# Performance work log

Measured on AMD Instinct MI355X. Metric: run time of the kernel, lower is better.

The kernel has to match this reference:

```python
import jax, jax.numpy as jnp
import numpy as np

N = 20000   # nodes
E = 320000  # edges
H = 4       # attention heads
GAT_SLOPE = 0.2   # DGL GATv2Conv internal leaky_relu slope
ACT_SLOPE = 0.01  # nn.LeakyReLU default slope


def gatv2_layer(h, src, dst, Wl, Wr, attn, b):
    """DGL GATv2Conv (share_weights=False, bias=True, eval mode).
    h: [N, Fin]; Wl/Wr: [Fin, H*D]; attn: [H, D]; b: [H*D]. Returns [N, H, D]."""
    n = h.shape[0]
    Hh, D = attn.shape
    fs = (h @ Wl).reshape(n, Hh, D)  # source projection
    fd = (h @ Wr).reshape(n, Hh, D)  # destination projection
    # edge-wise GATv2 score: a^T leaky_relu(Wl h_u + Wr h_v)
    e = jax.nn.leaky_relu(fs[src] + fd[dst], negative_slope=GAT_SLOPE)  # [E,H,D]
    logit = jnp.einsum('ehd,hd->eh', e, attn)  # [E,H]
    # edge softmax over incoming edges of each dst node (numerically stable)
    m = jax.ops.segment_max(logit, dst, num_segments=n)
    a = jnp.exp(logit - m[dst])
    s = jax.ops.segment_sum(a, dst, num_segments=n)
    alpha = a / s[dst]  # [E,H]
    out = jax.ops.segment_sum(alpha[:, :, None] * fs[src], dst, num_segments=n)
    return out + b.reshape(1, Hh, D)


def setup_inputs() -> dict:
    key = jax.random.key(0)
    ks = jax.random.split(key, 16)

    def w(k, shape, fan_in):
        return (jax.random.normal(k, shape, jnp.float32) / np.float32(np.sqrt(fan_in)))

    return {
        'n_feat': jax.random.normal(ks[0], (N, 512), jnp.float32),
        'src': jax.random.randint(ks[1], (E,), 0, N, jnp.int32),
        'dst': jax.random.randint(ks[2], (E,), 0, N, jnp.int32),
        # layer 0: 512 -> H x 128
        'Wl0': w(ks[3], (512, H * 128), 512), 'Wr0': w(ks[4], (512, H * 128), 512),
        'attn0': w(ks[5], (H, 128), 128), 'b0': jnp.zeros((H * 128,), jnp.float32),
        # layer 1: 128 -> H x 128
        'Wl1': w(ks[6], (128, H * 128), 128), 'Wr1': w(ks[7], (128, H * 128), 128),
        'attn1': w(ks[8], (H, 128), 128), 'b1': jnp.zeros((H * 128,), jnp.float32),
        # layer 2 (output): 128 -> H x 64
        'Wl2': w(ks[9], (128, H * 64), 128), 'Wr2': w(ks[10], (128, H * 64), 128),
        'attn2': w(ks[11], (H, 64), 64), 'b2': jnp.zeros((H * 64,), jnp.float32),
    }


def reference(n_feat, src, dst, Wl0, Wr0, attn0, b0, Wl1, Wr1, attn1, b1,
              Wl2, Wr2, attn2, b2):
    h = n_feat.reshape(n_feat.shape[0], -1)  # nn.Flatten
    for (Wl, Wr, attn, b) in ((Wl0, Wr0, attn0, b0),
                              (Wl1, Wr1, attn1, b1),
                              (Wl2, Wr2, attn2, b2)):
        h = gatv2_layer(h, src, dst, Wl, Wr, attn, b)  # [N,H,D]
        h = h.mean(axis=1)                              # head mean
        h = jax.nn.leaky_relu(h, negative_slope=ACT_SLOPE)
    # dgl.mean_nodes: per-graph mean readout (single graph -> [1, out])
    return h.mean(axis=0, keepdims=True)
```

## Files before the change

### kernel.cpp

```cpp
#include <hip/hip_runtime.h>
#include <hip/hip_bf16.h>
#include <stdint.h>


#define GAT_SLOPE 0.2f
#define ACT_SLOPE 0.01f
#define MAXDEG 64

typedef _Float16 half8 __attribute__((ext_vector_type(8)));
typedef _Float16 v2h __attribute__((ext_vector_type(2)));
typedef float floatx4 __attribute__((ext_vector_type(4)));

struct TransDesc {
  const float* src;
  _Float16* dst;
  int K, M, off;
};
struct PreArgs {
  TransDesc d[6];
  int wTotal;
  const float* nf;
  _Float16* A0;
  int aTotal;
  const int* src;
  const int* dst;
  int* counts;
  int* pcsrc;
  int E;
};

__global__ __launch_bounds__(256) void preproc_kernel(PreArgs pa) {
  int i = blockIdx.x * 256 + threadIdx.x;
  const int total = pa.wTotal + pa.aTotal + pa.E;
  if (i >= total) return;
  if (i < pa.wTotal) {
    int q = 0;
#pragma unroll
    for (int j = 1; j < 6; ++j)
      if (i >= pa.d[j].off) q = j;
    int local = i - pa.d[q].off;
    int K = pa.d[q].K, M = pa.d[q].M;
    int m = local / K, k = local % K;
    pa.d[q].dst[local] = (_Float16)pa.d[q].src[(size_t)k * M + m];
  } else if (i < pa.wTotal + pa.aTotal) {
    int j = i - pa.wTotal;
    pa.A0[j] = (_Float16)pa.nf[j];
  } else {
    int e = i - pa.wTotal - pa.aTotal;
    int d = pa.dst[e];
    int pos = atomicAdd(&pa.counts[d], 1);
    if (pos < MAXDEG) pa.pcsrc[(size_t)d * MAXDEG + pos] = pa.src[e];
  }
}

__device__ __forceinline__ void gload_lds16(const _Float16* g, _Float16* l) {
  __builtin_amdgcn_global_load_lds(
      (__attribute__((address_space(1))) unsigned int*)g,
      (__attribute__((address_space(3))) unsigned int*)l, 16, 0, 0);
}

#define TM 128
#define TN 128
#define TK 32

__global__ __launch_bounds__(256) void gemm_mfma_dual_kernel(
    const _Float16* __restrict__ A, const _Float16* __restrict__ B0,
    const _Float16* __restrict__ B1, _Float16* __restrict__ C0,
    _Float16* __restrict__ C1, int Nrow, int K, int M, int nStrips,
    int nbxLog2) {
  const int id = blockIdx.x;
  const int xcd = id & 7;
  const int s = id >> 3;
  const int nbx = 1 << nbxLog2;
  const int col = s & (nbx - 1);
  const int chunk = s >> nbxLog2;
  const int strip = chunk * 8 + xcd;
  if (strip >= nStrips) return;

  const int nb = nbx >> 1;
  const bool second = col >= nb;
  const _Float16* B = second ? B1 : B0;
  _Float16* C = second ? C1 : C0;
  const int bn = (second ? col - nb : col) * TN;
  const int bm = strip * TM;

  __shared__ __align__(16) _Float16 As[TM * TK];
  __shared__ __align__(16) _Float16 Bs[TN * TK];

  const int tid = threadIdx.x;
  const int w = tid >> 6;
  const int lane = tid & 63;
  const int wr = w >> 1;
  const int wc = w & 1;
  const int quad = lane >> 4;
  const int lr = lane & 15;

  const int lrow = lane >> 2;
  const int loff = (lane & 3) * 8;

  floatx4 acc[4][4];
#pragma unroll
  for (int i = 0; i < 4; ++i)
#pragma unroll
    for (int j = 0; j < 4; ++j) acc[i][j] = (floatx4){0.f, 0.f, 0.f, 0.f};

  const int KT = K / TK;
  for (int kt = 0; kt < KT; ++kt) {
    const int k0 = kt * TK;
#pragma unroll
    for (int half = 0; half < 2; ++half) {
      const int r0 = w * 32 + half * 16;
      int ga = bm + r0 + lrow;
      if (ga >= Nrow) ga = Nrow - 1;
      gload_lds16(A + (size_t)ga * K + k0 + loff, As + r0 * TK);
      gload_lds16(B + (size_t)(bn + r0 + lrow) * K + k0 + loff, Bs + r0 * TK);
    }
    __syncthreads();

    half8 ar[4], br[4];
#pragma unroll
    for (int i = 0; i < 4; ++i) {
      int row = wr * 64 + i * 16 + lr;
      ar[i] = *(const half8*)(As + row * TK + quad * 8);
    }
#pragma unroll
    for (int j = 0; j < 4; ++j) {
      int colr = wc * 64 + j * 16 + lr;
      br[j] = *(const half8*)(Bs + colr * TK + quad * 8);
    }
#pragma unroll
    for (int i = 0; i < 4; ++i)
#pragma unroll
      for (int j = 0; j < 4; ++j)
        acc[i][j] = __builtin_amdgcn_mfma_f32_16x16x32_f16(ar[i], br[j],
                                                           acc[i][j], 0, 0, 0);
    __syncthreads();
  }

#pragma unroll
  for (int i = 0; i < 4; ++i) {
#pragma unroll
    for (int r = 0; r < 4; ++r) {
      int row = bm + wr * 64 + i * 16 + quad * 4 + r;
      if (row >= Nrow) continue;
#pragma unroll
      for (int j = 0; j < 4; ++j) {
        int colc = bn + wc * 64 + j * 16 + lr;
        C[(size_t)row * M + colc] = (_Float16)acc[i][j][r];
      }
    }
  }
}

template <int D>
__global__ __launch_bounds__(128) void node_attn_kernel(
    const _Float16* __restrict__ fs, const _Float16* __restrict__ fd,
    const int* __restrict__ counts, const int* __restrict__ pcsrc,
    const float* __restrict__ attn, const float* __restrict__ bias,
    float* __restrict__ hout, _Float16* __restrict__ oh, int N) {
  constexpr int HD = 4 * D;
  constexpr int R = HD / 64;
  constexpr int R2 = R / 2;
  typedef _Float16 halfR __attribute__((ext_vector_type(R)));
  union Frag {
    halfR v;
    v2h h[R2];
    _Float16 s[R];
  };
  const int v = blockIdx.x;
  if (v >= N) return;
  const int wid = threadIdx.x >> 6;
  const int lane = threadIdx.x & 63;

  const v2h slope2 = {(_Float16)GAT_SLOPE, (_Float16)GAT_SLOPE};

  Frag fdv;
  fdv.v = *(const halfR*)(fd + (size_t)v * HD + lane * R);
  v2h ar2[R2];
#pragma unroll
  for (int j = 0; j < R2; ++j) {
    ar2[j][0] = (_Float16)attn[lane * R + 2 * j];
    ar2[j][1] = (_Float16)attn[lane * R + 2 * j + 1];
  }

  float m = -INFINITY, l = 0.f;
  float O[R];
#pragma unroll
  for (int i = 0; i < R; ++i) O[i] = 0.f;

  const int cnt = min(counts[v], MAXDEG);
  const int* elist = pcsrc + (size_t)v * MAXDEG;
  const int mid = (cnt + 1) >> 1;
  int k = wid ? mid : 0;
  const int ke = wid ? cnt : mid;

  for (; k + 3 < ke; k += 4) {
    const int s0 = elist[k];
    const int s1 = elist[k + 1];
    const int s2 = elist[k + 2];
    const int s3 = elist[k + 3];
    Frag t0, t1, t2, t3;
    t0.v = *(const halfR*)(fs + (size_t)s0 * HD + lane * R);
    t1.v = *(const halfR*)(fs + (size_t)s1 * HD + lane * R);
    t2.v = *(const halfR*)(fs + (size_t)s2 * HD + lane * R);
    t3.v = *(const halfR*)(fs + (size_t)s3 * HD + lane * R);
    float p0 = 0.f, p1 = 0.f, p2 = 0.f, p3 = 0.f;
#pragma unroll
    for (int j = 0; j < R2; ++j) {
      v2h x0 = t0.h[j] + fdv.h[j];
      v2h x1 = t1.h[j] + fdv.h[j];
      v2h x2 = t2.h[j] + fdv.h[j];
      v2h x3 = t3.h[j] + fdv.h[j];
      x0 = __builtin_elementwise_max(x0, x0 * slope2);
      x1 = __builtin_elementwise_max(x1, x1 * slope2);
      x2 = __builtin_elementwise_max(x2, x2 * slope2);
      x3 = __builtin_elementwise_max(x3, x3 * slope2);
      p0 = __builtin_amdgcn_fdot2(ar2[j], x0, p0, false);
      p1 = __builtin_amdgcn_fdot2(ar2[j], x1, p1, false);
      p2 = __builtin_amdgcn_fdot2(ar2[j], x2, p2, false);
      p3 = __builtin_amdgcn_fdot2(ar2[j], x3, p3, false);
    }
#pragma unroll
    for (int off = 1; off <= 8; off <<= 1) {
      p0 += __shfl_xor(p0, off, 64);
      p1 += __shfl_xor(p1, off, 64);
      p2 += __shfl_xor(p2, off, 64);
      p3 += __shfl_xor(p3, off, 64);
    }
    const float mq = fmaxf(fmaxf(p0, p1), fmaxf(p2, p3));
    const float w0 = __expf(p0 - mq);
    const float w1 = __expf(p1 - mq);
    const float w2 = __expf(p2 - mq);
    const float w3 = __expf(p3 - mq);
    const float mnew = fmaxf(m, mq);
    const float sc = __expf(m - mnew);
    const float sq = __expf(mq - mnew);
    l = l * sc + (w0 + w1 + w2 + w3) * sq;
#pragma unroll
    for (int i = 0; i < R; ++i) {
      float acc = (float)t0.s[i] * w0;
      acc = fmaf((float)t1.s[i], w1, acc);
      acc = fmaf((float)t2.s[i], w2, acc);
      acc = fmaf((float)t3.s[i], w3, acc);
      O[i] = fmaf(O[i], sc, sq * acc);
    }
    m = mnew;
  }
  for (; k < ke; ++k) {
    const int s0 = elist[k];
    Frag t0;
    t0.v = *(const halfR*)(fs + (size_t)s0 * HD + lane * R);
    float p0 = 0.f;
#pragma unroll
    for (int j = 0; j < R2; ++j) {
      v2h x0 = t0.h[j] + fdv.h[j];
      x0 = __builtin_elementwise_max(x0, x0 * slope2);
      p0 = __builtin_amdgcn_fdot2(ar2[j], x0, p0, false);
    }
#pragma unroll
    for (int off = 1; off <= 8; off <<= 1) p0 += __shfl_xor(p0, off, 64);
    const float mnew = fmaxf(m, p0);
    const float sc = __expf(m - mnew);
    const float p = __expf(p0 - mnew);
    l = l * sc + p;
#pragma unroll
    for (int i = 0; i < R; ++i) O[i] = fmaf(O[i], sc, p * (float)t0.s[i]);
    m = mnew;
  }

  __shared__ float sO[64 * R];
  __shared__ float sM[64];
  __shared__ float sL[64];
  if (wid == 1) {
    sM[lane] = m;
    sL[lane] = l;
#pragma unroll
    for (int i = 0; i < R; ++i) sO[lane * R + i] = O[i];
  }
  __syncthreads();
  if (wid == 1) return;
  {
    const float m1 = sM[lane];
    const float l1 = sL[lane];
    const float mstar = fmaxf(m, m1);
    const float a0 = (l > 0.f) ? __expf(m - mstar) : 0.f;
    const float a1 = (l1 > 0.f) ? __expf(m1 - mstar) : 0.f;
    l = l * a0 + l1 * a1;
#pragma unroll
    for (int i = 0; i < R; ++i) O[i] = O[i] * a0 + sO[lane * R + i] * a1;
  }

  const float inv = (l > 0.f) ? 1.f / l : 0.f;
#pragma unroll
  for (int i = 0; i < R; ++i) O[i] = O[i] * inv + bias[lane * R + i];
#pragma unroll
  for (int i = 0; i < R; ++i) {
    O[i] += __shfl_xor(O[i], 16, 64);
    O[i] += __shfl_xor(O[i], 32, 64);
    float x = O[i] * 0.25f;
    O[i] = x > 0.f ? x : x * ACT_SLOPE;
  }
  if (lane < 16) {
    const size_t base = (size_t)v * D + lane * R;
    if (hout) {
#pragma unroll
      for (int i = 0; i < R; ++i) hout[base + i] = O[i];
    }
    if (oh) {
#pragma unroll
      for (int i = 0; i < R; ++i) oh[base + i] = (_Float16)O[i];
    }
  }
}

__global__ __launch_bounds__(64) void final_mean_kernel(
    const float* __restrict__ h, float* __restrict__ out, int N) {
  const int d = threadIdx.x;
  float acc = 0.f;
  for (int n = blockIdx.x; n < N; n += gridDim.x) acc += h[(size_t)n * 64 + d];
  atomicAdd(&out[d], acc / (float)N);
}

extern "C" void kernel_launch(void* const* d_in, const int* in_sizes, int n_in,
                              void* d_out, int out_size, void* d_ws,
                              size_t ws_size, hipStream_t stream) {
  const float* n_feat = (const float*)d_in[0];
  const int* src = (const int*)d_in[1];
  const int* dst = (const int*)d_in[2];
  const float* Wl[3] = {(const float*)d_in[3], (const float*)d_in[7],
                        (const float*)d_in[11]};
  const float* Wr[3] = {(const float*)d_in[4], (const float*)d_in[8],
                        (const float*)d_in[12]};
  const float* attn[3] = {(const float*)d_in[5], (const float*)d_in[9],
                          (const float*)d_in[13]};
  const float* bias[3] = {(const float*)d_in[6], (const float*)d_in[10],
                          (const float*)d_in[14]};

  const int N = in_sizes[0] / 512;
  const int E = in_sizes[1];
  const int Kdim[3] = {512, 128, 128};
  const int Mdim[3] = {512, 512, 256};

  char* ws = (char*)d_ws;
  size_t o = 0;
  auto alloc = [&](size_t bytes) {
    void* p = ws + o;
    o += (bytes + 15) & ~(size_t)15;
    return p;
  };
  _Float16* fs = (_Float16*)alloc((size_t)N * 512 * 2);
  _Float16* fd = (_Float16*)alloc((size_t)N * 512 * 2);
  _Float16* A0 = (_Float16*)alloc((size_t)N * 512 * 2);
  _Float16* h1 = (_Float16*)alloc((size_t)N * 128 * 2);
  _Float16* h2 = (_Float16*)alloc((size_t)N * 128 * 2);
  float* hfin = (float*)alloc((size_t)N * 64 * 4);
  _Float16 *WlT[3], *WrT[3];
  for (int L = 0; L < 3; ++L) {
    size_t sz = (size_t)Kdim[L] * Mdim[L] * 2;
    WlT[L] = (_Float16*)alloc(sz);
    WrT[L] = (_Float16*)alloc(sz);
  }
  int* counts = (int*)alloc((size_t)N * 4);
  int* pcsrc = (int*)alloc((size_t)N * MAXDEG * 4);

  hipMemsetAsync(counts, 0, (size_t)N * sizeof(int), stream);
  {
    PreArgs pa;
    int off = 0;
    for (int L = 0; L < 3; ++L) {
      pa.d[2 * L] = {Wl[L], WlT[L], Kdim[L], Mdim[L], off};
      off += Kdim[L] * Mdim[L];
      pa.d[2 * L + 1] = {Wr[L], WrT[L], Kdim[L], Mdim[L], off};
      off += Kdim[L] * Mdim[L];
    }
    pa.wTotal = off;
    pa.nf = n_feat;
    pa.A0 = A0;
    pa.aTotal = N * 512;
    pa.src = src;
    pa.dst = dst;
    pa.counts = counts;
    pa.pcsrc = pcsrc;
    pa.E = E;
    int total = pa.wTotal + pa.aTotal + pa.E;
    preproc_kernel<<<(total + 255) / 256, 256, 0, stream>>>(pa);
  }

  const _Float16* Ain[3] = {A0, h1, h2};

  const int nStrips = (N + TM - 1) / TM;
  const int S8 = ((nStrips + 7) / 8) * 8;

  for (int L = 0; L < 3; ++L) {
    const int K = Kdim[L], M = Mdim[L];
    const int nbx = 2 * M / TN;
    const int nbxLog2 = (nbx == 8) ? 3 : 2;
    gemm_mfma_dual_kernel<<<S8 * nbx, 256, 0, stream>>>(
        Ain[L], WlT[L], WrT[L], fs, fd, N, K, M, nStrips, nbxLog2);
    if (L == 0) {
      node_attn_kernel<128><<<N, 128, 0, stream>>>(fs, fd, counts, pcsrc,
                                                   attn[L], bias[L], nullptr,
                                                   h1, N);
    } else if (L == 1) {
      node_attn_kernel<128><<<N, 128, 0, stream>>>(fs, fd, counts, pcsrc,
                                                   attn[L], bias[L], nullptr,
                                                   h2, N);
    } else {
      node_attn_kernel<64><<<N, 128, 0, stream>>>(fs, fd, counts, pcsrc,
                                                  attn[L], bias[L], hfin,
                                                  nullptr, N);
    }
  }

  hipMemsetAsync(d_out, 0, 64 * sizeof(float), stream);
  final_mean_kernel<<<256, 64, 0, stream>>>(hfin, (float*)d_out, N);
}
```

Baseline: 357.6 us.

## Fuse whole GATv2 pipeline into one cooperative persistent kernel with grid syncs

Replaces the separate preprocess, GEMM, attention and final-mean launches with a single cooperative mega-kernel whose stages are separated by grid.sync, with the counts and output zeroing folded into the preprocessing stage instead of memsets. The attention stage now handles one node per wave (four per block) instead of splitting one node across two waves, and the last layer reduces the node mean into shared memory and atomics, dropping the hfin buffer and the final kernel. The aim is to remove launch gaps and intermediate traffic. In exchange the GEMM and attention stages run on a fixed persistent grid capped at 768 blocks, and grid-wide barriers add sync cost. A multi-kernel fallback path is kept.

```diff
diff --git a/kernel.cpp b/kernel.cpp
--- a/kernel.cpp
+++ b/kernel.cpp
@@ -1,23 +1,26 @@
 #include <hip/hip_runtime.h>
+#include <hip/hip_cooperative_groups.h>
 #include <hip/hip_bf16.h>
 #include <stdint.h>
+
+namespace cg = cooperative_groups;
 
 
 #define GAT_SLOPE 0.2f
 #define ACT_SLOPE 0.01f
 #define MAXDEG 64
+#define TM 128
+#define TN 128
+#define TK 32
 
 typedef _Float16 half8 __attribute__((ext_vector_type(8)));
 typedef _Float16 v2h __attribute__((ext_vector_type(2)));
 typedef float floatx4 __attribute__((ext_vector_type(4)));
 
-struct TransDesc {
-  const float* src;
-  _Float16* dst;
-  int K, M, off;
-};
-struct PreArgs {
-  TransDesc d[6];
+struct MegaArgs {
+  const float* W[6];
+  _Float16* WT[6];
+  int wK[6], wM[6], wOff[6];
   int wTotal;
   const float* nf;
   _Float16* A0;
@@ -27,31 +30,19 @@
   int* counts;
   int* pcsrc;
   int E;
+  float* dout;
+  const _Float16* Ain[3];
+  const _Float16* Bl[3];
+  const _Float16* Br[3];
+  _Float16* fs;
+  _Float16* fd;
+  _Float16* oh[2];
+  const float* aw[3];
+  const float* bias[3];
+  int Kd[3], Md[3], tiles[3], nbxL[3];
+  int nStrips;
+  int N;
 };
-
-__global__ __launch_bounds__(256) void preproc_kernel(PreArgs pa) {
-  int i = blockIdx.x * 256 + threadIdx.x;
-  const int total = pa.wTotal + pa.aTotal + pa.E;
-  if (i >= total) return;
-  if (i < pa.wTotal) {
-    int q = 0;
-#pragma unroll
-    for (int j = 1; j < 6; ++j)
-      if (i >= pa.d[j].off) q = j;
-    int local = i - pa.d[q].off;
-    int K = pa.d[q].K, M = pa.d[q].M;
-    int m = local / K, k = local % K;
-    pa.d[q].dst[local] = (_Float16)pa.d[q].src[(size_t)k * M + m];
-  } else if (i < pa.wTotal + pa.aTotal) {
-    int j = i - pa.wTotal;
-    pa.A0[j] = (_Float16)pa.nf[j];
-  } else {
-    int e = i - pa.wTotal - pa.aTotal;
-    int d = pa.dst[e];
-    int pos = atomicAdd(&pa.counts[d], 1);
-    if (pos < MAXDEG) pa.pcsrc[(size_t)d * MAXDEG + pos] = pa.src[e];
-  }
-}
 
 __device__ __forceinline__ void gload_lds16(const _Float16* g, _Float16* l) {
   __builtin_amdgcn_global_load_lds(
@@ -59,34 +50,44 @@
       (__attribute__((address_space(3))) unsigned int*)l, 16, 0, 0);
 }
 
-#define TM 128
-#define TN 128
-#define TK 32
-
-__global__ __launch_bounds__(256) void gemm_mfma_dual_kernel(
-    const _Float16* __restrict__ A, const _Float16* __restrict__ B0,
-    const _Float16* __restrict__ B1, _Float16* __restrict__ C0,
-    _Float16* __restrict__ C1, int Nrow, int K, int M, int nStrips,
-    int nbxLog2) {
-  const int id = blockIdx.x;
-  const int xcd = id & 7;
-  const int s = id >> 3;
-  const int nbx = 1 << nbxLog2;
-  const int col = s & (nbx - 1);
-  const int chunk = s >> nbxLog2;
-  const int strip = chunk * 8 + xcd;
-  if (strip >= nStrips) return;
-
-  const int nb = nbx >> 1;
-  const bool second = col >= nb;
-  const _Float16* B = second ? B1 : B0;
-  _Float16* C = second ? C1 : C0;
-  const int bn = (second ? col - nb : col) * TN;
-  const int bm = strip * TM;
-
-  __shared__ __align__(16) _Float16 As[TM * TK];
-  __shared__ __align__(16) _Float16 Bs[TN * TK];
-
+__device__ void pre_stage(const MegaArgs& a) {
+  const int total = a.wTotal + a.aTotal + a.N + 64;
+  for (int i = blockIdx.x * 256 + threadIdx.x; i < total;
+       i += gridDim.x * 256) {
+    if (i < a.wTotal) {
+      int q = 0;
+#pragma unroll
+      for (int j = 1; j < 6; ++j)
+        if (i >= a.wOff[j]) q = j;
+      int local = i - a.wOff[q];
+      int K = a.wK[q], M = a.wM[q];
+      int m = local / K, k = local % K;
+      a.WT[q][local] = (_Float16)a.W[q][(size_t)k * M + m];
+    } else if (i < a.wTotal + a.aTotal) {
+      int j = i - a.wTotal;
+      a.A0[j] = (_Float16)a.nf[j];
+    } else if (i < a.wTotal + a.aTotal + a.N) {
+      a.counts[i - a.wTotal - a.aTotal] = 0;
+    } else {
+      a.dout[i - a.wTotal - a.aTotal - a.N] = 0.f;
+    }
+  }
+}
+
+__device__ void scatter_stage(const MegaArgs& a) {
+  for (int e = blockIdx.x * 256 + threadIdx.x; e < a.E; e += gridDim.x * 256) {
+    int d = a.dst[e];
+    int pos = atomicAdd(&a.counts[d], 1);
+    if (pos < MAXDEG) a.pcsrc[(size_t)d * MAXDEG + pos] = a.src[e];
+  }
+}
+
+__device__ void gemm_stage(const _Float16* __restrict__ A,
+                           const _Float16* __restrict__ B0,
+                           const _Float16* __restrict__ B1,
+                           _Float16* __restrict__ C0, _Float16* __restrict__ C1,
+                           int Nrow, int K, int M, int nStrips, int nbxLog2,
+                           int totalTiles, _Float16* As, _Float16* Bs) {
   const int tid = threadIdx.x;
   const int w = tid >> 6;
   const int lane = tid & 63;
@@ -94,70 +95,90 @@
   const int wc = w & 1;
   const int quad = lane >> 4;
   const int lr = lane & 15;
-
   const int lrow = lane >> 2;
   const int loff = (lane & 3) * 8;
-
-  floatx4 acc[4][4];
-#pragma unroll
-  for (int i = 0; i < 4; ++i)
-#pragma unroll
-    for (int j = 0; j < 4; ++j) acc[i][j] = (floatx4){0.f, 0.f, 0.f, 0.f};
-
-  const int KT = K / TK;
-  for (int kt = 0; kt < KT; ++kt) {
-    const int k0 = kt * TK;
-#pragma unroll
-    for (int half = 0; half < 2; ++half) {
-      const int r0 = w * 32 + half * 16;
-      int ga = bm + r0 + lrow;
-      if (ga >= Nrow) ga = Nrow - 1;
-      gload_lds16(A + (size_t)ga * K + k0 + loff, As + r0 * TK);
-      gload_lds16(B + (size_t)(bn + r0 + lrow) * K + k0 + loff, Bs + r0 * TK);
+  const int nbx = 1 << nbxLog2;
+  const int nb = nbx >> 1;
+
+  for (int T = blockIdx.x; T < totalTiles; T += gridDim.x) {
+    const int xcd = T & 7;
+    const int s = T >> 3;
+    const int col = s & (nbx - 1);
+    const int chunk = s >> nbxLog2;
+    const int strip = chunk * 8 + xcd;
+    if (strip >= nStrips) continue;
+
+    const bool second = col >= nb;
+    const _Float16* B = second ? B1 : B0;
+    _Float16* C = second ? C1 : C0;
+    const int bn = (second ? col - nb : col) * TN;
+    const int bm = strip * TM;
+
+    floatx4 acc[4][4];
+#pragma unroll
+    for (int i = 0; i < 4; ++i)
+#pragma unroll
+      for (int j = 0; j < 4; ++j) acc[i][j] = (floatx4){0.f, 0.f, 0.f, 0.f};
+
+    const int KT = K / TK;
+    for (int kt = 0; kt < KT; ++kt) {
+      const int k0 = kt * TK;
+#pragma unroll
+      for (int half = 0; half < 2; ++half) {
+        const int r0 = w * 32 + half * 16;
+        int ga = bm + r0 + lrow;
+        if (ga >= Nrow) ga = Nrow - 1;
+        gload_lds16(A + (size_t)ga * K + k0 + loff, As + r0 * TK);
+        gload_lds16(B + (size_t)(bn + r0 + lrow) * K + k0 + loff,
+                    Bs + r0 * TK);
+      }
+      __syncthreads();
+
+      half8 ar[4], br[4];
+#pragma unroll
+      for (int i = 0; i < 4; ++i) {
+        int row = wr * 64 + i * 16 + lr;
+        ar[i] = *(const half8*)(As + row * TK + quad * 8);
+      }
+#pragma unroll
+      for (int j = 0; j < 4; ++j) {
+        int colr = wc * 64 + j * 16 + lr;
+        br[j] = *(const half8*)(Bs + colr * TK + quad * 8);
+      }
+#pragma unroll
+      for (int i = 0; i < 4; ++i)
+#pragma unroll
+        for (int j = 0; j < 4; ++j)
+          acc[i][j] = __builtin_amdgcn_mfma_f32_16x16x32_f16(
+              ar[i], br[j], acc[i][j], 0, 0, 0);
+      __syncthreads();
     }
-    __syncthreads();
-
-    half8 ar[4], br[4];
+
 #pragma unroll
     for (int i = 0; i < 4; ++i) {
-      int row = wr * 64 + i * 16 + lr;
-      ar[i] = *(const half8*)(As + row * TK + quad * 8);
+#pragma unroll
+      for (int r = 0; r < 4; ++r) {
+        int row = bm + wr * 64 + i * 16 + quad * 4 + r;
+        if (row >= Nrow) continue;
+#pragma unroll
+        for (int j = 0; j < 4; ++j) {
+          int colc = bn + wc * 64 + j * 16 + lr;
+          C[(size_t)row * M + colc] = (_Float16)acc[i][j][r];
+        }
+      }
     }
-#pragma unroll
-    for (int j = 0; j < 4; ++j) {
-      int colr = wc * 64 + j * 16 + lr;
-      br[j] = *(const half8*)(Bs + colr * TK + quad * 8);
-    }
-#pragma unroll
-    for (int i = 0; i < 4; ++i)
-#pragma unroll
-      for (int j = 0; j < 4; ++j)
-        acc[i][j] = __builtin_amdgcn_mfma_f32_16x16x32_f16(ar[i], br[j],
-                                                           acc[i][j], 0, 0, 0);
-    __syncthreads();
-  }
-
-#pragma unroll
-  for (int i = 0; i < 4; ++i) {
-#pragma unroll
-    for (int r = 0; r < 4; ++r) {
-      int row = bm + wr * 64 + i * 16 + quad * 4 + r;
-      if (row >= Nrow) continue;
-#pragma unroll
-      for (int j = 0; j < 4; ++j) {
-        int colc = bn + wc * 64 + j * 16 + lr;
-        C[(size_t)row * M + colc] = (_Float16)acc[i][j][r];
-      }
-    }
-  }
-}
-
-template <int D>
-__global__ __launch_bounds__(128) void node_attn_kernel(
-    const _Float16* __restrict__ fs, const _Float16* __restrict__ fd,
-    const int* __restrict__ counts, const int* __restrict__ pcsrc,
-    const float* __restrict__ attn, const float* __restrict__ bias,
-    float* __restrict__ hout, _Float16* __restrict__ oh, int N) {
+  }
+}
+
+template <int D, bool LAST>
+__device__ void attn_stage(const _Float16* __restrict__ fs,
+                           const _Float16* __restrict__ fd,
+                           const int* __restrict__ counts,
+                           const int* __restrict__ pcsrc,
+                           const float* __restrict__ aw,
+                           const float* __restrict__ bias,
+                           _Float16* __restrict__ oh, float* __restrict__ dout,
+                           int N, float* facc) {
   constexpr int HD = 4 * D;
   constexpr int R = HD / 64;
   constexpr int R2 = R / 2;
@@ -167,158 +188,193 @@
     v2h h[R2];
     _Float16 s[R];
   };
-  const int v = blockIdx.x;
-  if (v >= N) return;
   const int wid = threadIdx.x >> 6;
   const int lane = threadIdx.x & 63;
-
   const v2h slope2 = {(_Float16)GAT_SLOPE, (_Float16)GAT_SLOPE};
 
-  Frag fdv;
-  fdv.v = *(const halfR*)(fd + (size_t)v * HD + lane * R);
+  if (LAST) {
+    if (threadIdx.x < 64) facc[threadIdx.x] = 0.f;
+    __syncthreads();
+  }
+
   v2h ar2[R2];
 #pragma unroll
   for (int j = 0; j < R2; ++j) {
-    ar2[j][0] = (_Float16)attn[lane * R + 2 * j];
-    ar2[j][1] = (_Float16)attn[lane * R + 2 * j + 1];
-  }
-
-  float m = -INFINITY, l = 0.f;
-  float O[R];
-#pragma unroll
-  for (int i = 0; i < R; ++i) O[i] = 0.f;
-
-  const int cnt = min(counts[v], MAXDEG);
-  const int* elist = pcsrc + (size_t)v * MAXDEG;
-  const int mid = (cnt + 1) >> 1;
-  int k = wid ? mid : 0;
-  const int ke = wid ? cnt : mid;
-
-  for (; k + 3 < ke; k += 4) {
-    const int s0 = elist[k];
-    const int s1 = elist[k + 1];
-    const int s2 = elist[k + 2];
-    const int s3 = elist[k + 3];
-    Frag t0, t1, t2, t3;
-    t0.v = *(const halfR*)(fs + (size_t)s0 * HD + lane * R);
-    t1.v = *(const halfR*)(fs + (size_t)s1 * HD + lane * R);
-    t2.v = *(const halfR*)(fs + (size_t)s2 * HD + lane * R);
-    t3.v = *(const halfR*)(fs + (size_t)s3 * HD + lane * R);
-    float p0 = 0.f, p1 = 0.f, p2 = 0.f, p3 = 0.f;
-#pragma unroll
-    for (int j = 0; j < R2; ++j) {
-      v2h x0 = t0.h[j] + fdv.h[j];
-      v2h x1 = t1.h[j] + fdv.h[j];
-      v2h x2 = t2.h[j] + fdv.h[j];
-      v2h x3 = t3.h[j] + fdv.h[j];
-      x0 = __builtin_elementwise_max(x0, x0 * slope2);
-      x1 = __builtin_elementwise_max(x1, x1 * slope2);
-      x2 = __builtin_elementwise_max(x2, x2 * slope2);
-      x3 = __builtin_elementwise_max(x3, x3 * slope2);
-      p0 = __builtin_amdgcn_fdot2(ar2[j], x0, p0, false);
-      p1 = __builtin_amdgcn_fdot2(ar2[j], x1, p1, false);
-      p2 = __builtin_amdgcn_fdot2(ar2[j], x2, p2, false);
-      p3 = __builtin_amdgcn_fdot2(ar2[j], x3, p3, false);
+    ar2[j][0] = (_Float16)aw[lane * R + 2 * j];
+    ar2[j][1] = (_Float16)aw[lane * R + 2 * j + 1];
+  }
+  float br[R];
+#pragma unroll
+  for (int i = 0; i < R; ++i) br[i] = bias[lane * R + i];
+
+  for (int v0 = blockIdx.x * 4; v0 < N; v0 += gridDim.x * 4) {
+    const int v = v0 + wid;
+    if (v < N) {
+      Frag fdv;
+      fdv.v = *(const halfR*)(fd + (size_t)v * HD + lane * R);
+      float m = -INFINITY, l = 0.f;
+      float O[R];
+#pragma unroll
+      for (int i = 0; i < R; ++i) O[i] = 0.f;
+
+      const int cnt = min(counts[v], MAXDEG);
+      const int* elist = pcsrc + (size_t)v * MAXDEG;
+      int k = 0;
+      for (; k + 3 < cnt; k += 4) {
+        const int s0 = elist[k];
+        const int s1 = elist[k + 1];
+        const int s2 = elist[k + 2];
+        const int s3 = elist[k + 3];
+        Frag t0, t1, t2, t3;
+        t0.v = *(const halfR*)(fs + (size_t)s0 * HD + lane * R);
+        t1.v = *(const halfR*)(fs + (size_t)s1 * HD + lane * R);
+        t2.v = *(const halfR*)(fs + (size_t)s2 * HD + lane * R);
+        t3.v = *(const halfR*)(fs + (size_t)s3 * HD + lane * R);
+        float p0 = 0.f, p1 = 0.f, p2 = 0.f, p3 = 0.f;
+#pragma unroll
+        for (int j = 0; j < R2; ++j) {
+          v2h x0 = t0.h[j] + fdv.h[j];
+          v2h x1 = t1.h[j] + fdv.h[j];
+          v2h x2 = t2.h[j] + fdv.h[j];
+          v2h x3 = t3.h[j] + fdv.h[j];
+          x0 = __builtin_elementwise_max(x0, x0 * slope2);
+          x1 = __builtin_elementwise_max(x1, x1 * slope2);
+          x2 = __builtin_elementwise_max(x2, x2 * slope2);
+          x3 = __builtin_elementwise_max(x3, x3 * slope2);
+          p0 = __builtin_amdgcn_fdot2(ar2[j], x0, p0, false);
+          p1 = __builtin_amdgcn_fdot2(ar2[j], x1, p1, false);
+          p2 = __builtin_amdgcn_fdot2(ar2[j], x2, p2, false);
+          p3 = __builtin_amdgcn_fdot2(ar2[j], x3, p3, false);
+        }
+#pragma unroll
+        for (int off = 1; off <= 8; off <<= 1) {
+          p0 += __shfl_xor(p0, off, 64);
+          p1 += __shfl_xor(p1, off, 64);
+          p2 += __shfl_xor(p2, off, 64);
+          p3 += __shfl_xor(p3, off, 64);
+        }
+        const float mq = fmaxf(fmaxf(p0, p1), fmaxf(p2, p3));
+        const float w0 = __expf(p0 - mq);
+        const float w1 = __expf(p1 - mq);
+        const float w2 = __expf(p2 - mq);
+        const float w3 = __expf(p3 - mq);
+        const float mnew = fmaxf(m, mq);
+        const float sc = __expf(m - mnew);
+        const float sq = __expf(mq - mnew);
+        l = l * sc + (w0 + w1 + w2 + w3) * sq;
+#pragma unroll
+        for (int i = 0; i < R; ++i) {
+          float acc = (float)t0.s[i] * w0;
+          acc = fmaf((float)t1.s[i], w1, acc);
+          acc = fmaf((float)t2.s[i], w2, acc);
+          acc = fmaf((float)t3.s[i], w3, acc);
+          O[i] = fmaf(O[i], sc, sq * acc);
+        }
+        m = mnew;
+      }
+      for (; k < cnt; ++k) {
+        const int s0 = elist[k];
+        Frag t0;
+        t0.v = *(const halfR*)(fs + (size_t)s0 * HD + lane * R);
+        float p0 = 0.f;
+#pragma unroll
+        for (int j = 0; j < R2; ++j) {
+          v2h x0 = t0.h[j] + fdv.h[j];
+          x0 = __builtin_elementwise_max(x0, x0 * slope2);
+          p0 = __builtin_amdgcn_fdot2(ar2[j], x0, p0, false);
+        }
+#pragma unroll
+        for (int off = 1; off <= 8; off <<= 1) p0 += __shfl_xor(p0, off, 64);
+        const float mnew = fmaxf(m, p0);
+        const float sc = __expf(m - mnew);
+        const float p = __expf(p0 - mnew);
+        l = l * sc + p;
+#pragma unroll
+        for (int i = 0; i < R; ++i) O[i] = fmaf(O[i], sc, p * (float)t0.s[i]);
+        m = mnew;
+      }
+
+      const float inv = (l > 0.f) ? 1.f / l : 0.f;
+#pragma unroll
+      for (int i = 0; i < R; ++i) O[i] = O[i] * inv + br[i];
+#pragma unroll
+      for (int i = 0; i < R; ++i) {
+        O[i] += __shfl_xor(O[i], 16, 64);
+        O[i] += __shfl_xor(O[i], 32, 64);
+        float x = O[i] * 0.25f;
+        O[i] = x > 0.f ? x : x * ACT_SLOPE;
+      }
+      if (lane < 16) {
+        if (!LAST) {
+          const size_t base = (size_t)v * D + lane * R;
+#pragma unroll
+          for (int i = 0; i < R; ++i) oh[base + i] = (_Float16)O[i];
+        } else {
+#pragma unroll
+          for (int i = 0; i < R; ++i) atomicAdd(&facc[lane * R + i], O[i]);
+        }
+      }
     }
-#pragma unroll
-    for (int off = 1; off <= 8; off <<= 1) {
-      p0 += __shfl_xor(p0, off, 64);
-      p1 += __shfl_xor(p1, off, 64);
-      p2 += __shfl_xor(p2, off, 64);
-      p3 += __shfl_xor(p3, off, 64);
-    }
-    const float mq = fmaxf(fmaxf(p0, p1), fmaxf(p2, p3));
-    const float w0 = __expf(p0 - mq);
-    const float w1 = __expf(p1 - mq);
-    const float w2 = __expf(p2 - mq);
-    const float w3 = __expf(p3 - mq);
-    const float mnew = fmaxf(m, mq);
-    const float sc = __expf(m - mnew);
-    const float sq = __expf(mq - mnew);
-    l = l * sc + (w0 + w1 + w2 + w3) * sq;
-#pragma unroll
-    for (int i = 0; i < R; ++i) {
-      float acc = (float)t0.s[i] * w0;
-      acc = fmaf((float)t1.s[i], w1, acc);
-      acc = fmaf((float)t2.s[i], w2, acc);
-      acc = fmaf((float)t3.s[i], w3, acc);
-      O[i] = fmaf(O[i], sc, sq * acc);
-    }
-    m = mnew;
-  }
-  for (; k < ke; ++k) {
-    const int s0 = elist[k];
-    Frag t0;
-    t0.v = *(const halfR*)(fs + (size_t)s0 * HD + lane * R);
-    float p0 = 0.f;
-#pragma unroll
-    for (int j = 0; j < R2; ++j) {
-      v2h x0 = t0.h[j] + fdv.h[j];
-      x0 = __builtin_elementwise_max(x0, x0 * slope2);
-      p0 = __builtin_amdgcn_fdot2(ar2[j], x0, p0, false);
-    }
-#pragma unroll
-    for (int off = 1; off <= 8; off <<= 1) p0 += __shfl_xor(p0, off, 64);
-    const float mnew = fmaxf(m, p0);
-    const float sc = __expf(m - mnew);
-    const float p = __expf(p0 - mnew);
-    l = l * sc + p;
-#pragma unroll
-    for (int i = 0; i < R; ++i) O[i] = fmaf(O[i], sc, p * (float)t0.s[i]);
-    m = mnew;
-  }
-
-  __shared__ float sO[64 * R];
-  __shared__ float sM[64];
-  __shared__ float sL[64];
-  if (wid == 1) {
-    sM[lane] = m;
-    sL[lane] = l;
-#pragma unroll
-    for (int i = 0; i < R; ++i) sO[lane * R + i] = O[i];
-  }
-  __syncthreads();
-  if (wid == 1) return;
-  {
-    const float m1 = sM[lane];
-    const float l1 = sL[lane];
-    const float mstar = fmaxf(m, m1);
-    const float a0 = (l > 0.f) ? __expf(m - mstar) : 0.f;
-    const float a1 = (l1 > 0.f) ? __expf(m1 - mstar) : 0.f;
-    l = l * a0 + l1 * a1;
-#pragma unroll
-    for (int i = 0; i < R; ++i) O[i] = O[i] * a0 + sO[lane * R + i] * a1;
-  }
-
-  const float inv = (l > 0.f) ? 1.f / l : 0.f;
-#pragma unroll
-  for (int i = 0; i < R; ++i) O[i] = O[i] * inv + bias[lane * R + i];
-#pragma unroll
-  for (int i = 0; i < R; ++i) {
-    O[i] += __shfl_xor(O[i], 16, 64);
-    O[i] += __shfl_xor(O[i], 32, 64);
-    float x = O[i] * 0.25f;
-    O[i] = x > 0.f ? x : x * ACT_SLOPE;
-  }
-  if (lane < 16) {
-    const size_t base = (size_t)v * D + lane * R;
-    if (hout) {
-#pragma unroll
-      for (int i = 0; i < R; ++i) hout[base + i] = O[i];
-    }
-    if (oh) {
-#pragma unroll
-      for (int i = 0; i < R; ++i) oh[base + i] = (_Float16)O[i];
-    }
-  }
-}
-
-__global__ __launch_bounds__(64) void final_mean_kernel(
-    const float* __restrict__ h, float* __restrict__ out, int N) {
-  const int d = threadIdx.x;
-  float acc = 0.f;
-  for (int n = blockIdx.x; n < N; n += gridDim.x) acc += h[(size_t)n * 64 + d];
-  atomicAdd(&out[d], acc / (float)N);
+  }
+
+  if (LAST) {
+    __syncthreads();
+    if (threadIdx.x < 64)
+      atomicAdd(&dout[threadIdx.x], facc[threadIdx.x] / (float)N);
+  }
+}
+
+__global__ __launch_bounds__(256, 3) void mega_kernel(MegaArgs a) {
+  cg::grid_group grid = cg::this_grid();
+  __shared__ __align__(16) _Float16 As[TM * TK];
+  __shared__ __align__(16) _Float16 Bs[TN * TK];
+
+  pre_stage(a);
+  grid.sync();
+  scatter_stage(a);
+  grid.sync();
+
+  float* facc = (float*)As;
+
+  gemm_stage(a.Ain[0], a.Bl[0], a.Br[0], a.fs, a.fd, a.N, a.Kd[0], a.Md[0],
+             a.nStrips, a.nbxL[0], a.tiles[0], As, Bs);
+  grid.sync();
+  attn_stage<128, false>(a.fs, a.fd, a.counts, a.pcsrc, a.aw[0], a.bias[0],
+                         a.oh[0], nullptr, a.N, nullptr);
+  grid.sync();
+  gemm_stage(a.Ain[1], a.Bl[1], a.Br[1], a.fs, a.fd, a.N, a.Kd[1], a.Md[1],
+             a.nStrips, a.nbxL[1], a.tiles[1], As, Bs);
+  grid.sync();
+  attn_stage<128, false>(a.fs, a.fd, a.counts, a.pcsrc, a.aw[1], a.bias[1],
+                         a.oh[1], nullptr, a.N, nullptr);
+  grid.sync();
+  gemm_stage(a.Ain[2], a.Bl[2], a.Br[2], a.fs, a.fd, a.N, a.Kd[2], a.Md[2],
+             a.nStrips, a.nbxL[2], a.tiles[2], As, Bs);
+  grid.sync();
+  attn_stage<64, true>(a.fs, a.fd, a.counts, a.pcsrc, a.aw[2], a.bias[2],
+                       nullptr, a.dout, a.N, facc);
+}
+
+__global__ __launch_bounds__(256) void pre_kernel(MegaArgs a) { pre_stage(a); }
+__global__ __launch_bounds__(256) void scatter_kernel(MegaArgs a) {
+  scatter_stage(a);
+}
+__global__ __launch_bounds__(256) void gemm_fb_kernel(
+    const _Float16* A, const _Float16* B0, const _Float16* B1, _Float16* C0,
+    _Float16* C1, int Nrow, int K, int M, int nStrips, int nbxLog2,
+    int totalTiles) {
+  __shared__ __align__(16) _Float16 As[TM * TK];
+  __shared__ __align__(16) _Float16 Bs[TN * TK];
+  gemm_stage(A, B0, B1, C0, C1, Nrow, K, M, nStrips, nbxLog2, totalTiles, As,
+             Bs);
+}
+template <int D, bool LAST>
+__global__ __launch_bounds__(256) void attn_fb_kernel(
+    const _Float16* fs, const _Float16* fd, const int* counts,
+    const int* pcsrc, const float* aw, const float* bias, _Float16* oh,
+    float* dout, int N) {
+  __shared__ float facc[64];
+  attn_stage<D, LAST>(fs, fd, counts, pcsrc, aw, bias, oh, dout, N, facc);
 }
 
 extern "C" void kernel_launch(void* const* d_in, const int* in_sizes, int n_in,
@@ -331,8 +387,8 @@
                         (const float*)d_in[11]};
   const float* Wr[3] = {(const float*)d_in[4], (const float*)d_in[8],
                         (const float*)d_in[12]};
-  const float* attn[3] = {(const float*)d_in[5], (const float*)d_in[9],
-                          (const float*)d_in[13]};
+  const float* attnw[3] = {(const float*)d_in[5], (const float*)d_in[9],
+                           (const float*)d_in[13]};
   const float* bias[3] = {(const float*)d_in[6], (const float*)d_in[10],
                           (const float*)d_in[14]};
 
@@ -353,65 +409,108 @@
   _Float16* A0 = (_Float16*)alloc((size_t)N * 512 * 2);
   _Float16* h1 = (_Float16*)alloc((size_t)N * 128 * 2);
   _Float16* h2 = (_Float16*)alloc((size_t)N * 128 * 2);
-  float* hfin = (float*)alloc((size_t)N * 64 * 4);
-  _Float16 *WlT[3], *WrT[3];
+  _Float16* WT[6];
   for (int L = 0; L < 3; ++L) {
     size_t sz = (size_t)Kdim[L] * Mdim[L] * 2;
-    WlT[L] = (_Float16*)alloc(sz);
-    WrT[L] = (_Float16*)alloc(sz);
+    WT[2 * L] = (_Float16*)alloc(sz);
+    WT[2 * L + 1] = (_Float16*)alloc(sz);
   }
   int* counts = (int*)alloc((size_t)N * 4);
   int* pcsrc = (int*)alloc((size_t)N * MAXDEG * 4);
 
-  hipMemsetAsync(counts, 0, (size_t)N * sizeof(int), stream);
+  MegaArgs a;
   {
-    PreArgs pa;
     int off = 0;
     for (int L = 0; L < 3; ++L) {
-      pa.d[2 * L] = {Wl[L], WlT[L], Kdim[L], Mdim[L], off};
+      a.W[2 * L] = Wl[L];
+      a.W[2 * L + 1] = Wr[L];
+      a.WT[2 * L] = WT[2 * L];
+      a.WT[2 * L + 1] = WT[2 * L + 1];
+      a.wK[2 * L] = a.wK[2 * L + 1] = Kdim[L];
+      a.wM[2 * L] = a.wM[2 * L + 1] = Mdim[L];
+      a.wOff[2 * L] = off;
       off += Kdim[L] * Mdim[L];
-      pa.d[2 * L + 1] = {Wr[L], WrT[L], Kdim[L], Mdim[L], off};
+      a.wOff[2 * L + 1] = off;
       off += Kdim[L] * Mdim[L];
     }
-    pa.wTotal = off;
-    pa.nf = n_feat;
-    pa.A0 = A0;
-    pa.aTotal = N * 512;
-    pa.src = src;
-    pa.dst = dst;
-    pa.counts = counts;
-    pa.pcsrc = pcsrc;
-    pa.E = E;
-    int total = pa.wTotal + pa.aTotal + pa.E;
-    preproc_kernel<<<(total + 255) / 256, 256, 0, stream>>>(pa);
-  }
-
-  const _Float16* Ain[3] = {A0, h1, h2};
-
-  const int nStrips = (N + TM - 1) / TM;
-  const int S8 = ((nStrips + 7) / 8) * 8;
-
+    a.wTotal = off;
+  }
+  a.nf = n_feat;
+  a.A0 = A0;
+  a.aTotal = N * 512;
+  a.src = src;
+  a.dst = dst;
+  a.counts = counts;
+  a.pcsrc = pcsrc;
+  a.E = E;
+  a.dout = (float*)d_out;
+  a.Ain[0] = A0;
+  a.Ain[1] = h1;
+  a.Ain[2] = h2;
   for (int L = 0; L < 3; ++L) {
-    const int K = Kdim[L], M = Mdim[L];
-    const int nbx = 2 * M / TN;
-    const int nbxLog2 = (nbx == 8) ? 3 : 2;
-    gemm_mfma_dual_kernel<<<S8 * nbx, 256, 0, stream>>>(
-        Ain[L], WlT[L], WrT[L], fs, fd, N, K, M, nStrips, nbxLog2);
-    if (L == 0) {
-      node_attn_kernel<128><<<N, 128, 0, stream>>>(fs, fd, counts, pcsrc,
-                                                   attn[L], bias[L], nullptr,
-                                                   h1, N);
-    } else if (L == 1) {
-      node_attn_kernel<128><<<N, 128, 0, stream>>>(fs, fd, counts, pcsrc,
-                                                   attn[L], bias[L], nullptr,
-                                                   h2, N);
-    } else {
-      node_attn_kernel<64><<<N, 128, 0, stream>>>(fs, fd, counts, pcsrc,
-                                                  attn[L], bias[L], hfin,
-                                                  nullptr, N);
+    a.Bl[L] = WT[2 * L];
+    a.Br[L] = WT[2 * L + 1];
+    a.Kd[L] = Kdim[L];
+    a.Md[L] = Mdim[L];
+    a.aw[L] = attnw[L];
+    a.bias[L] = bias[L];
+  }
+  a.fs = fs;
+  a.fd = fd;
+  a.oh[0] = h1;
+  a.oh[1] = h2;
+  a.nStrips = (N + TM - 1) / TM;
+  const int S8 = ((a.nStrips + 7) / 8) * 8;
+  a.nbxL[0] = 3;
+  a.nbxL[1] = 3;
+  a.nbxL[2] = 2;
+  a.tiles[0] = S8 * 8;
+  a.tiles[1] = S8 * 8;
+  a.tiles[2] = S8 * 4;
+  a.N = N;
+
+  auto run_fallback = [&]() {
+    int totalPre = a.wTotal + a.aTotal + a.N + 64;
+    pre_kernel<<<(totalPre + 255) / 256, 256, 0, stream>>>(a);
+    scatter_kernel<<<(E + 255) / 256, 256, 0, stream>>>(a);
+    for (int L = 0; L < 3; ++L) {
+      gemm_fb_kernel<<<a.tiles[L], 256, 0, stream>>>(
+          a.Ain[L], a.Bl[L], a.Br[L], fs, fd, N, a.Kd[L], a.Md[L], a.nStrips,
+          a.nbxL[L], a.tiles[L]);
+      if (L == 0) {
+        attn_fb_kernel<128, false><<<(N + 3) / 4, 256, 0, stream>>>(
+            fs, fd, counts, pcsrc, a.aw[0], a.bias[0], h1, nullptr, N);
+      } else if (L == 1) {
+        attn_fb_kernel<128, false><<<(N + 3) / 4, 256, 0, stream>>>(
+            fs, fd, counts, pcsrc, a.aw[1], a.bias[1], h2, nullptr, N);
+      } else {
+        attn_fb_kernel<64, true><<<(N + 3) / 4, 256, 0, stream>>>(
+            fs, fd, counts, pcsrc, a.aw[2], a.bias[2], nullptr, (float*)d_out,
+            N);
+      }
     }
-  }
-
-  hipMemsetAsync(d_out, 0, 64 * sizeof(float), stream);
-  final_mean_kernel<<<256, 64, 0, stream>>>(hfin, (float*)d_out, N);
-}
+  };
+
+  int dev = 0;
+  (void)hipGetDevice(&dev);
+  int coopAttr = 0;
+  (void)hipDeviceGetAttribute(&coopAttr, hipDeviceAttributeCooperativeLaunch,
+                              dev);
+  int occ = 0;
+  hipError_t oe =
+      hipOccupancyMaxActiveBlocksPerMultiprocessor(&occ, mega_kernel, 256, 0);
+  int nblk = 0;
+  if (oe == hipSuccess && occ > 0) {
+    nblk = occ * 256;
+    if (nblk > 768) nblk = 768;
+    nblk &= ~7;
+  }
+  bool launched = false;
+  if (coopAttr && nblk >= 8) {
+    void* params[] = {&a};
+    hipError_t le = hipLaunchCooperativeKernel(mega_kernel, dim3(nblk),
+                                               dim3(256), params, 0, stream);
+    launched = (le == hipSuccess);
+  }
+  if (!launched) run_fallback();
+}
```

Result: slower. 898.8 us (+151.3%).
